# Optimization experiments

Hardware: AMD Instinct MI355X
Metric: run time of the kernel (lower is better)

Reference implementation:

```python
import jax, jax.numpy as jnp
import numpy as np

C = 768; NH = 12; HD = 64; WS = 14; VPT = 10; H0 = 64; B = 8
SCALE = HD ** -0.5


def layernorm(x, w, b, eps=1e-5):
    m = x.mean(-1, keepdims=True)
    v = x.var(-1, keepdims=True)
    return (x - m) / jnp.sqrt(v + eps) * w + b


def setup_inputs() -> dict:
    key = jax.random.key(0)
    ks = jax.random.split(key, 8)
    def rn(k, shape, s=0.02):
        return jax.random.normal(k, shape, jnp.float32) * s
    L = VPT + H0 * H0
    return {
        "x": jax.random.normal(ks[0], (B, L, C), jnp.float32),
        "ln1_w": jnp.ones((C,), jnp.float32),
        "ln1_b": jnp.zeros((C,), jnp.float32),
        "qkv_w": rn(ks[1], (3 * C, C)),
        "qkv_b": jnp.zeros((3 * C,), jnp.float32),
        "proj_w": rn(ks[2], (C, C)),
        "proj_b": jnp.zeros((C,), jnp.float32),
        "rel_pos_h": rn(ks[3], (2 * WS - 1, HD)),
        "rel_pos_w": rn(ks[4], (2 * WS - 1, HD)),
        "ln2_w": jnp.ones((C,), jnp.float32),
        "ln2_b": jnp.zeros((C,), jnp.float32),
        "mlp_w1": rn(ks[5], (4 * C, C)),
        "mlp_b1": jnp.zeros((4 * C,), jnp.float32),
        "mlp_w2": rn(ks[6], (C, 4 * C)),
        "mlp_b2": jnp.zeros((C,), jnp.float32),
        "H": H0,
        "W": H0,
    }


def reference(x, ln1_w, ln1_b, qkv_w, qkv_b, proj_w, proj_b, rel_pos_h, rel_pos_w,
              ln2_w, ln2_b, mlp_w1, mlp_b1, mlp_w2, mlp_b2, H, W):
    B_, L, C_ = x.shape
    shortcut = x
    xn = layernorm(x, ln1_w, ln1_b)

    # --- window partition (SAM style, pad bottom/right) ---
    prompt = xn[:, :VPT]                           # (B, VPT, C)
    sp = xn[:, VPT:].reshape(B_, H, W, C_)
    pad_h = (WS - H % WS) % WS
    pad_w = (WS - W % WS) % WS
    Hp, Wp = H + pad_h, W + pad_w
    sp = jnp.pad(sp, ((0, 0), (0, pad_h), (0, pad_w), (0, 0)))
    nh, nw = Hp // WS, Wp // WS
    win = sp.reshape(B_, nh, WS, nw, WS, C_).transpose(0, 1, 3, 2, 4, 5)
    win = win.reshape(-1, WS * WS, C_)             # (B*nwin, WS*WS, C), batch-major
    nwin = nh * nw
    # faithful to original: prompts broadcast window-major, windows are batch-major
    pr = jnp.broadcast_to(prompt[None], (nwin, B_, VPT, C_)).reshape(-1, VPT, C_)
    tok = jnp.concatenate([pr, win], axis=1)       # (Bw, Lw, C)
    Bw, Lw, _ = tok.shape

    # --- attention with decomposed rel-pos ---
    qkv = tok @ qkv_w.T + qkv_b
    qkv = qkv.reshape(Bw, Lw, 3, NH, HD).transpose(2, 0, 3, 1, 4).reshape(3, Bw * NH, Lw, HD)
    q, k, v = qkv[0], qkv[1], qkv[2]
    attn = (q * SCALE) @ k.transpose(0, 2, 1)      # (Bw*NH, Lw, Lw)

    coords = jnp.arange(WS)[:, None] - jnp.arange(WS)[None, :] + (WS - 1)
    Rh = rel_pos_h[coords]                         # (WS, WS, HD)
    Rw = rel_pos_w[coords]
    rq = q[:, VPT:].reshape(Bw * NH, WS, WS, HD)
    rel_h = jnp.einsum('bhwc,hkc->bhwk', rq, Rh)
    rel_w = jnp.einsum('bhwc,wkc->bhwk', rq, Rw)
    ori = attn[:, VPT:, VPT:].reshape(-1, WS, WS, WS, WS)
    ori = ori + rel_h[:, :, :, :, None] + rel_w[:, :, :, None, :]
    attn = attn.at[:, VPT:, VPT:].set(ori.reshape(-1, WS * WS, WS * WS))

    attn = jax.nn.softmax(attn, axis=-1)
    out = (attn @ v).reshape(Bw, NH, Lw, HD).transpose(0, 2, 1, 3).reshape(Bw, Lw, C_)
    out = out @ proj_w.T + proj_b

    # --- window unpartition ---
    pr_out = out[:, :VPT].reshape(nwin, B_, VPT, C_).mean(0)   # (B, VPT, C)
    wo = out[:, VPT:].reshape(B_, nh, nw, WS, WS, C_).transpose(0, 1, 3, 2, 4, 5)
    wo = wo.reshape(B_, Hp, Wp, C_)[:, :H, :W].reshape(B_, H * W, C_)
    x2 = jnp.concatenate([pr_out, wo], axis=1)

    x2 = shortcut + x2
    h = layernorm(x2, ln2_w, ln2_b)
    h = jax.nn.gelu(h @ mlp_w1.T + mlp_b1, approximate=False)
    x2 = x2 + (h @ mlp_w2.T + mlp_b2)
    return x2
```

## Files before the change

### kernel.cpp

```cpp
#include <hip/hip_runtime.h>
#include <hip/hip_fp16.h>

#define Bb 8
#define Ll 4106
#define Cc 768
#define VPT_ 10
#define WSz 14
#define NWIN 25
#define BW_ 200
#define LW_ 206
#define NHh 12
#define HDd 64

typedef _Float16 half8 __attribute__((ext_vector_type(8)));
typedef float floatx4 __attribute__((ext_vector_type(4)));

__device__ __forceinline__ void gload16(const _Float16* g, _Float16* l) {
    __builtin_amdgcn_global_load_lds(
        (const __attribute__((address_space(1))) void*)g,
        (__attribute__((address_space(3))) void*)l, 16, 0, 0);
}

__global__ void f2h_kernel(const float* __restrict__ in, _Float16* __restrict__ out, int n) {
    int i = blockIdx.x * 256 + threadIdx.x;
    if (i < n) out[i] = (_Float16)in[i];
}

__global__ __launch_bounds__(256) void ln1_kernel(
    const float* __restrict__ x, const float* __restrict__ w, const float* __restrict__ bia,
    _Float16* __restrict__ xn)
{
    int r = blockIdx.x;
    const float* xr = x + (size_t)r * Cc;
    int t = threadIdx.x;
    float v0 = xr[t], v1 = xr[t + 256], v2 = xr[t + 512];
    float s1 = v0 + v1 + v2;
    float s2 = v0 * v0 + v1 * v1 + v2 * v2;
    #pragma unroll
    for (int off = 32; off > 0; off >>= 1) {
        s1 += __shfl_down(s1, off);
        s2 += __shfl_down(s2, off);
    }
    __shared__ float red[8];
    int wv = t >> 6, ln = t & 63;
    if (ln == 0) { red[wv] = s1; red[4 + wv] = s2; }
    __syncthreads();
    float fs1 = red[0] + red[1] + red[2] + red[3];
    float fs2 = red[4] + red[5] + red[6] + red[7];
    float mean = fs1 * (1.0f / Cc);
    float var  = fs2 * (1.0f / Cc) - mean * mean;
    float rstd = rsqrtf(var + 1e-5f);
    float vv[3] = {v0, v1, v2};
    #pragma unroll
    for (int i = 0; i < 3; ++i) {
        int c = t + i * 256;
        xn[(size_t)r * Cc + c] = (_Float16)((vv[i] - mean) * rstd * w[c] + bia[c]);
    }
}

__global__ __launch_bounds__(256) void ln2_kernel(
    const _Float16* __restrict__ x2, const float* __restrict__ w, const float* __restrict__ bia,
    _Float16* __restrict__ xn)
{
    int r = blockIdx.x;
    const _Float16* xr = x2 + (size_t)r * Cc;
    int t = threadIdx.x;
    float v0 = (float)xr[t], v1 = (float)xr[t + 256], v2 = (float)xr[t + 512];
    float s1 = v0 + v1 + v2;
    float s2 = v0 * v0 + v1 * v1 + v2 * v2;
    #pragma unroll
    for (int off = 32; off > 0; off >>= 1) {
        s1 += __shfl_down(s1, off);
        s2 += __shfl_down(s2, off);
    }
    __shared__ float red[8];
    int wv = t >> 6, ln = t & 63;
    if (ln == 0) { red[wv] = s1; red[4 + wv] = s2; }
    __syncthreads();
    float fs1 = red[0] + red[1] + red[2] + red[3];
    float fs2 = red[4] + red[5] + red[6] + red[7];
    float mean = fs1 * (1.0f / Cc);
    float var  = fs2 * (1.0f / Cc) - mean * mean;
    float rstd = rsqrtf(var + 1e-5f);
    float vv[3] = {v0, v1, v2};
    #pragma unroll
    for (int i = 0; i < 3; ++i) {
        int c = t + i * 256;
        xn[(size_t)r * Cc + c] = (_Float16)((vv[i] - mean) * rstd * w[c] + bia[c]);
    }
}

__global__ __launch_bounds__(256) void pmean_kernel(
    const _Float16* __restrict__ attP, _Float16* __restrict__ attS)
{
    int r = blockIdx.x;
    int b = r / VPT_, l = r % VPT_;
    int t = threadIdx.x;
    #pragma unroll
    for (int i = 0; i < 3; ++i) {
        int c = t + i * 256;
        float s = 0.0f;
        for (int wi = 0; wi < NWIN; ++wi)
            s += (float)attP[((size_t)((wi * Bb + b) * VPT_ + l)) * Cc + c];
        attS[((size_t)(b * Ll + l)) * Cc + c] = (_Float16)(s * (1.0f / NWIN));
    }
}

template <int EPI>
__global__ __launch_bounds__(256) void gemm128(
    const _Float16* __restrict__ A, const _Float16* __restrict__ W,
    const float* __restrict__ bias, const _Float16* __restrict__ addsrc,
    const float* __restrict__ addF,
    _Float16* __restrict__ outH, float* __restrict__ outF,
    int M, int N, int K, int gm, int gn)
{
    __shared__ alignas(16) _Float16 As[128 * 32];
    __shared__ alignas(16) _Float16 Bs[128 * 32];

    int pid = blockIdx.x;
    int width = 8 * gn;
    int gid = pid / width;
    int first = gid * 8;
    int gsz = gm - first; if (gsz > 8) gsz = 8;
    int rem = pid - gid * width;
    int pm = first + rem % gsz;
    int pn = rem / gsz;
    int row0 = pm * 128, col0 = pn * 128;

    int tid = threadIdx.x;
    int wv = tid >> 6, ln = tid & 63;
    int n = ln & 15, quad = ln >> 4;
    int wr = wv >> 1, wc = wv & 1;
    int lr = ln >> 2, lg = ln & 3;

    int lsw = (lg ^ ((lr >> 1) & 3)) * 8;
    int ar0 = row0 + wv * 16 + lr;        if (ar0 > M - 1) ar0 = M - 1;
    int ar1 = row0 + (wv + 4) * 16 + lr;  if (ar1 > M - 1) ar1 = M - 1;
    const _Float16* Ap0 = A + (size_t)ar0 * K + lsw;
    const _Float16* Ap1 = A + (size_t)ar1 * K + lsw;
    const _Float16* Bp0 = W + (size_t)(col0 + wv * 16 + lr) * K + lsw;
    const _Float16* Bp1 = W + (size_t)(col0 + (wv + 4) * 16 + lr) * K + lsw;
    _Float16* lA0 = As + wv * 512;
    _Float16* lA1 = As + (wv + 4) * 512;
    _Float16* lB0 = Bs + wv * 512;
    _Float16* lB1 = Bs + (wv + 4) * 512;

    const int cq = (quad ^ ((n >> 1) & 3)) * 8;

    floatx4 acc[4][4] = {};

    for (int k0 = 0; k0 < K; k0 += 32) {
        __syncthreads();
        gload16(Ap0 + k0, lA0);
        gload16(Ap1 + k0, lA1);
        gload16(Bp0 + k0, lB0);
        gload16(Bp1 + k0, lB1);
        __syncthreads();
        half8 af[4], bf[4];
        #pragma unroll
        for (int i = 0; i < 4; ++i)
            af[i] = *reinterpret_cast<const half8*>(&As[(wr * 64 + i * 16 + n) * 32 + cq]);
        #pragma unroll
        for (int j = 0; j < 4; ++j)
            bf[j] = *reinterpret_cast<const half8*>(&Bs[(wc * 64 + j * 16 + n) * 32 + cq]);
        #pragma unroll
        for (int i = 0; i < 4; ++i)
            #pragma unroll
            for (int j = 0; j < 4; ++j)
                acc[i][j] = __builtin_amdgcn_mfma_f32_16x16x32_f16(af[i], bf[j], acc[i][j], 0, 0, 0);
    }

    float bv[4];
    #pragma unroll
    for (int j = 0; j < 4; ++j) bv[j] = bias[col0 + wc * 64 + j * 16 + n];

    if (EPI == 2) {
        #pragma unroll
        for (int i = 0; i < 4; ++i)
            #pragma unroll
            for (int j = 0; j < 4; ++j) {
                int col = col0 + wc * 64 + j * 16 + n;
                #pragma unroll
                for (int rr = 0; rr < 4; ++rr) {
                    int row = row0 + wr * 64 + i * 16 + quad * 4 + rr;
                    if (row < M) {
                        size_t off = (size_t)row * N + col;
                        outF[off] = acc[i][j][rr] + bv[j] + (float)addsrc[off];
                    }
                }
            }
    } else if (EPI == 3) {
        #pragma unroll
        for (int i = 0; i < 4; ++i)
            #pragma unroll
            for (int j = 0; j < 4; ++j) {
                int col = col0 + wc * 64 + j * 16 + n;
                #pragma unroll
                for (int rr = 0; rr < 4; ++rr) {
                    int row = row0 + wr * 64 + i * 16 + quad * 4 + rr;
                    if (row < M) {
                        size_t off = (size_t)row * N + col;
                        outH[off] = (_Float16)(acc[i][j][rr] + bv[j] + addF[off]);
                    }
                }
            }
    } else {
        __syncthreads();
        _Float16* Tb = (wv < 2 ? As : Bs) + (wv & 1) * 2048;
        #pragma unroll
        for (int i = 0; i < 4; ++i) {
            #pragma unroll
            for (int j = 0; j < 4; ++j)
                #pragma unroll
                for (int rr = 0; rr < 4; ++rr) {
                    float v = acc[i][j][rr] + bv[j];
                    if (EPI == 1) v = 0.5f * v * (1.0f + erff(v * 0.70710678118654752f));
                    Tb[(quad * 4 + rr) * 72 + j * 16 + n] = (_Float16)v;
                }
            __syncthreads();
            int row = row0 + wr * 64 + i * 16 + lr;
            if (row < M) {
                uint4 p0 = *reinterpret_cast<const uint4*>(&Tb[lr * 72 + lg * 8]);
                uint4 p1 = *reinterpret_cast<const uint4*>(&Tb[lr * 72 + 32 + lg * 8]);
                _Float16* po = outH + (size_t)row * N + col0 + wc * 64 + lg * 8;
                *reinterpret_cast<uint4*>(po) = p0;
                *reinterpret_cast<uint4*>(po + 32) = p1;
            }
        }
    }
}

__global__ __launch_bounds__(256, 2) void attn_mfma_kernel(
    const _Float16* __restrict__ qkv, const _Float16* __restrict__ qkvbh,
    const float* __restrict__ relh, const float* __restrict__ relw,
    _Float16* __restrict__ attS, _Float16* __restrict__ attP)
{
    __shared__ alignas(16) _Float16 Ks[208 * 72];
    __shared__ alignas(16) _Float16 Vt[64 * 232];
    __shared__ alignas(16) _Float16 Pc[4][16 * 40];
    __shared__ alignas(16) float    Tabs[4][896];
    __shared__ int rowOff[208];
    const int bwi = blockIdx.x / NHh, hh = blockIdx.x % NHh;
    const int tid = threadIdx.x;

    const int bp = bwi & 7;
    const int bs = bwi / NWIN;
    const int wis = bwi % NWIN;
    const int wh = wis / 5, ww = wis % 5;

    const int wv = tid >> 6, ln = tid & 63;
    const int n = ln & 15, quad = ln >> 4;

    if (tid < 208) {
        int row = tid, off = -1;
        if (row < VPT_) off = bp * Ll + row;
        else if (row < LW_) {
            int s = row - VPT_;
            int i = s / WSz, j = s - i * WSz;
            int gi = wh * WSz + i, gj = ww * WSz + j;
            if (gi < 64 && gj < 64) off = bs * Ll + VPT_ + gi * 64 + gj;
        }
        rowOff[row] = off;
    }

    half8 bh[2][2], bwf[2][2];
    #pragma unroll
    for (int ct = 0; ct < 2; ++ct) {
        int j = ct * 16 + n; if (j > 26) j = 26;
        #pragma unroll
        for (int kk = 0; kk < 2; ++kk) {
            const float* ph = relh + j * 64 + kk * 32 + quad * 8;
            const float* pw = relw + j * 64 + kk * 32 + quad * 8;
            half8 hf, wf;
            #pragma unroll
            for (int e = 0; e < 8; ++e) { hf[e] = (_Float16)ph[e]; wf[e] = (_Float16)pw[e]; }
            bh[ct][kk] = hf; bwf[ct][kk] = wf;
        }
    }

    int khv[13], kwv[13];
    #pragma unroll
    for (int ct = 0; ct < 13; ++ct) {
        int key = ct * 16 + n;
        int k2 = key - VPT_; if (k2 < 0) k2 = 0;
        khv[ct] = k2 / WSz; kwv[ct] = k2 - khv[ct] * WSz;
    }
    __syncthreads();

    half8 qa0, qa1;
    {
        int qrow = wv * 16 + n; if (qrow > 205) qrow = 205;
        int ro = rowOff[qrow];
        const _Float16* qp = (ro >= 0 ? qkv + (size_t)ro * 2304 : qkvbh) + hh * HDd + quad * 8;
        qa0 = *reinterpret_cast<const half8*>(qp);
        qa1 = *reinterpret_cast<const half8*>(qp + 32);
    }

    for (int idx = tid; idx < LW_ * 8; idx += 256) {
        int row = idx >> 3, c8 = idx & 7;
        int ro = rowOff[row];
        const _Float16* src = (ro >= 0 ? qkv + (size_t)ro * 2304 : qkvbh) + 768 + hh * HDd;
        *reinterpret_cast<uint4*>(&Ks[row * 72 + c8 * 8]) =
            *reinterpret_cast<const uint4*>(src + c8 * 8);
    }
    for (int idx = tid; idx < LW_ * 64; idx += 256) {
        int row = idx >> 6, d = idx & 63;
        int ro = rowOff[row];
        const _Float16* src = (ro >= 0 ? qkv + (size_t)ro * 2304 : qkvbh) + 1536 + hh * HDd;
        Vt[d * 232 + row] = src[d];
    }
    for (int idx = tid; idx < 64 * 26; idx += 256) {
        int d = idx / 26, c = idx - d * 26;
        Vt[d * 232 + 206 + c] = (_Float16)0.0f;
    }
    __syncthreads();

    float* tw_t = Tabs[wv];
    float* th_t = Tabs[wv] + 448;
    _Float16* pcw = &Pc[wv][0];

    for (int rt = wv; rt < 13; rt += 4) {
        int nrt = rt + 4; if (nrt > 12) nrt = 12;
        int nqrow = nrt * 16 + n; if (nqrow > 205) nqrow = 205;
        int nro = rowOff[nqrow];
        const _Float16* nqp = (nro >= 0 ? qkv + (size_t)nro * 2304 : qkvbh) + hh * HDd + quad * 8;
        half8 nq0 = *reinterpret_cast<const half8*>(nqp);
        half8 nq1 = *reinterpret_cast<const half8*>(nqp + 32);

        floatx4 th0 = {}, th1 = {}, tw0 = {}, tw1 = {};
        th0 = __builtin_amdgcn_mfma_f32_16x16x32_f16(qa0, bh[0][0], th0, 0, 0, 0);
        th0 = __builtin_amdgcn_mfma_f32_16x16x32_f16(qa1, bh[0][1], th0, 0, 0, 0);
        th1 = __builtin_amdgcn_mfma_f32_16x16x32_f16(qa0, bh[1][0], th1, 0, 0, 0);
        th1 = __builtin_amdgcn_mfma_f32_16x16x32_f16(qa1, bh[1][1], th1, 0, 0, 0);
        tw0 = __builtin_amdgcn_mfma_f32_16x16x32_f16(qa0, bwf[0][0], tw0, 0, 0, 0);
        tw0 = __builtin_amdgcn_mfma_f32_16x16x32_f16(qa1, bwf[0][1], tw0, 0, 0, 0);
        tw1 = __builtin_amdgcn_mfma_f32_16x16x32_f16(qa0, bwf[1][0], tw1, 0, 0, 0);
        tw1 = __builtin_amdgcn_mfma_f32_16x16x32_f16(qa1, bwf[1][1], tw1, 0, 0, 0);

        #pragma unroll
        for (int rr = 0; rr < 4; ++rr) {
            int lrow = quad * 4 + rr;
            th_t[lrow * 28 + n] = th0[rr];
            tw_t[lrow * 28 + n] = tw0[rr];
            if (n < 12) {
                th_t[lrow * 28 + 16 + n] = th1[rr];
                tw_t[lrow * 28 + 16 + n] = tw1[rr];
            }
        }

        floatx4 s[13];
        #pragma unroll
        for (int ct = 0; ct < 13; ++ct) {
            half8 kb0 = *reinterpret_cast<const half8*>(&Ks[(ct * 16 + n) * 72 + quad * 8]);
            half8 kb1 = *reinterpret_cast<const half8*>(&Ks[(ct * 16 + n) * 72 + 32 + quad * 8]);
            floatx4 a = {};
            a = __builtin_amdgcn_mfma_f32_16x16x32_f16(qa0, kb0, a, 0, 0, 0);
            a = __builtin_amdgcn_mfma_f32_16x16x32_f16(qa1, kb1, a, 0, 0, 0);
            s[ct] = a;
        }

        #pragma unroll
        for (int rr = 0; rr < 4; ++rr) {
            int row = rt * 16 + quad * 4 + rr;
            bool rowok = (row >= VPT_) && (row < LW_);
            int q2 = row - VPT_; if (q2 < 0) q2 = 0;
            int qh = q2 / WSz, qw = q2 - qh * WSz;
            const float* thr = th_t + (quad * 4 + rr) * 28;
            const float* twr = tw_t + (quad * 4 + rr) * 28;
            #pragma unroll
            for (int ct = 0; ct < 13; ++ct) {
                int key = ct * 16 + n;
                float tv = thr[qh - khv[ct] + 13] + twr[qw - kwv[ct] + 13];
                float sv = s[ct][rr] * 0.125f;
                sv += (rowok && key >= VPT_ && key < LW_) ? tv : 0.0f;
                if (key >= LW_) sv = -1e30f;
                s[ct][rr] = sv;
            }
        }

        float mx[4] = {-1e30f, -1e30f, -1e30f, -1e30f};
        #pragma unroll
        for (int ct = 0; ct < 13; ++ct)
            #pragma unroll
            for (int rr = 0; rr < 4; ++rr) mx[rr] = fmaxf(mx[rr], s[ct][rr]);
        #pragma unroll
        for (int rr = 0; rr < 4; ++rr)
            #pragma unroll
            for (int off = 1; off < 16; off <<= 1) mx[rr] = fmaxf(mx[rr], __shfl_xor(mx[rr], off));
        float sm[4] = {0.f, 0.f, 0.f, 0.f};
        #pragma unroll
        for (int ct = 0; ct < 13; ++ct)
            #pragma unroll
            for (int rr = 0; rr < 4; ++rr) {
                float p = __expf(s[ct][rr] - mx[rr]);
                s[ct][rr] = p; sm[rr] += p;
            }
        #pragma unroll
        for (int rr = 0; rr < 4; ++rr) {
            #pragma unroll
            for (int off = 1; off < 16; off <<= 1) sm[rr] += __shfl_xor(sm[rr], off);
            sm[rr] = 1.0f / sm[rr];
        }
        #pragma unroll
        for (int ct = 0; ct < 13; ++ct)
            #pragma unroll
            for (int rr = 0; rr < 4; ++rr) s[ct][rr] *= sm[rr];

        floatx4 o[4] = {};
        #pragma unroll
        for (int kt = 0; kt < 7; ++kt) {
            #pragma unroll
            for (int h2 = 0; h2 < 2; ++h2) {
                int ct = kt * 2 + h2;
                #pragma unroll
                for (int rr = 0; rr < 4; ++rr) {
                    float pv = (ct < 13) ? s[ct][rr] : 0.0f;
                    pcw[(quad * 4 + rr) * 40 + h2 * 16 + n] = (_Float16)pv;
                }
            }
            half8 pa = *reinterpret_cast<const half8*>(&pcw[n * 40 + quad * 8]);
            #pragma unroll
            for (int dt = 0; dt < 4; ++dt) {
                half8 vb = *reinterpret_cast<const half8*>(&Vt[(dt * 16 + n) * 232 + kt * 32 + quad * 8]);
                o[dt] = __builtin_amdgcn_mfma_f32_16x16x32_f16(pa, vb, o[dt], 0, 0, 0);
            }
        }

        #pragma unroll
        for (int dt = 0; dt < 4; ++dt)
            #pragma unroll
            for (int rr = 0; rr < 4; ++rr) {
                int row = rt * 16 + quad * 4 + rr;
                if (row >= LW_) continue;
                _Float16 val = (_Float16)o[dt][rr];
                int col = hh * HDd + dt * 16 + n;
                if (row < VPT_) {
                    attP[((size_t)(bwi * VPT_ + row)) * Cc + col] = val;
                } else {
                    int g = rowOff[row];
                    if (g >= 0) attS[(size_t)g * Cc + col] = val;
                }
            }

        qa0 = nq0; qa1 = nq1;
    }
}

extern "C" void kernel_launch(void* const* d_in, const int* in_sizes, int n_in,
                              void* d_out, int out_size, void* d_ws, size_t ws_size,
                              hipStream_t stream)
{
    const float* x     = (const float*)d_in[0];
    const float* ln1w  = (const float*)d_in[1];
    const float* ln1b  = (const float*)d_in[2];
    const float* qkvw  = (const float*)d_in[3];
    const float* qkvb  = (const float*)d_in[4];
    const float* projw = (const float*)d_in[5];
    const float* projb = (const float*)d_in[6];
    const float* relh  = (const float*)d_in[7];
    const float* relw  = (const float*)d_in[8];
    const float* ln2w  = (const float*)d_in[9];
    const float* ln2b  = (const float*)d_in[10];
    const float* w1    = (const float*)d_in[11];
    const float* b1    = (const float*)d_in[12];
    const float* w2    = (const float*)d_in[13];
    const float* b2    = (const float*)d_in[14];
    float* out = (float*)d_out;
    char* ws = (char*)d_ws;

    _Float16* wqkv_h  = (_Float16*)(ws + 0);
    _Float16* wproj_h = (_Float16*)(ws + 3538944);
    _Float16* w1_h    = (_Float16*)(ws + 4718592);
    _Float16* w2_h    = (_Float16*)(ws + 9437184);
    _Float16* qkvb_h  = (_Float16*)(ws + 14155776);
    _Float16* attP    = (_Float16*)(ws + 14160384);
    _Float16* tokA    = (_Float16*)(ws + 17232384);
    char* regB = ws + 77438976;
    _Float16* qkv_h  = (_Float16*)regB;
    _Float16* hbuf   = (_Float16*)regB;
    _Float16* x2h    = (_Float16*)(regB + 100909056);

    f2h_kernel<<<(2304 * 768 + 255) / 256, 256, 0, stream>>>(qkvw, wqkv_h, 2304 * 768);
    f2h_kernel<<<(768 * 768 + 255) / 256, 256, 0, stream>>>(projw, wproj_h, 768 * 768);
    f2h_kernel<<<(3072 * 768 + 255) / 256, 256, 0, stream>>>(w1, w1_h, 3072 * 768);
    f2h_kernel<<<(768 * 3072 + 255) / 256, 256, 0, stream>>>(w2, w2_h, 768 * 3072);
    f2h_kernel<<<9, 256, 0, stream>>>(qkvb, qkvb_h, 2304);
    ln1_kernel<<<Bb * Ll, 256, 0, stream>>>(x, ln1w, ln1b, tokA);
    gemm128<0><<<257 * 18, 256, 0, stream>>>(tokA, wqkv_h, qkvb, nullptr, nullptr, qkv_h, nullptr,
                                             32848, 2304, 768, 257, 18);
    attn_mfma_kernel<<<BW_ * NHh, 256, 0, stream>>>(qkv_h, qkvb_h, relh, relw, tokA, attP);
    pmean_kernel<<<Bb * VPT_, 256, 0, stream>>>(attP, tokA);
    gemm128<3><<<257 * 6, 256, 0, stream>>>(tokA, wproj_h, projb, nullptr, x, x2h, nullptr,
                                            32848, 768, 768, 257, 6);
    ln2_kernel<<<Bb * Ll, 256, 0, stream>>>(x2h, ln2w, ln2b, tokA);
    for (int ch = 0; ch < 2; ++ch) {
        size_t r0 = (size_t)ch * 16424;
        gemm128<1><<<129 * 24, 256, 0, stream>>>(tokA + r0 * 768, w1_h, b1, nullptr, nullptr, hbuf, nullptr,
                                                 16424, 3072, 768, 129, 24);
        gemm128<2><<<129 * 6, 256, 0, stream>>>(hbuf, w2_h, b2, x2h + r0 * 768, nullptr, nullptr, out + r0 * 768,
                                                16424, 768, 3072, 129, 6);
    }
}
```

Before: 1.402 ms.

## Replace 128x128 GEMM with double-buffered 256x256 tile, 512-thread kernel

The GEMM moves from 128x128x32 tiles on 256 threads to 256x256x64 tiles on 512 threads, with double-buffered LDS (128 KB total) so the next K-slice is loaded while the current one is computed. Each wave now holds a 128x64 accumulator, which raises arithmetic intensity and halves the barriers per K. The cost is one block per CU, higher register pressure, and fewer blocks for the N=768 GEMMs (387 and 195 blocks), which can leave CUs idle and cause tail imbalance.

```diff
diff --git a/kernel.cpp b/kernel.cpp
--- a/kernel.cpp
+++ b/kernel.cpp
@@ -107,15 +107,14 @@
 }
 
 template <int EPI>
-__global__ __launch_bounds__(256) void gemm128(
+__global__ __launch_bounds__(512, 1) void gemm256(
     const _Float16* __restrict__ A, const _Float16* __restrict__ W,
     const float* __restrict__ bias, const _Float16* __restrict__ addsrc,
     const float* __restrict__ addF,
     _Float16* __restrict__ outH, float* __restrict__ outF,
     int M, int N, int K, int gm, int gn)
 {
-    __shared__ alignas(16) _Float16 As[128 * 32];
-    __shared__ alignas(16) _Float16 Bs[128 * 32];
+    __shared__ alignas(16) _Float16 AB[2][2][256 * 64];
 
     int pid = blockIdx.x;
     int width = 8 * gn;
@@ -125,64 +124,83 @@
     int rem = pid - gid * width;
     int pm = first + rem % gsz;
     int pn = rem / gsz;
-    int row0 = pm * 128, col0 = pn * 128;
+    int row0 = pm * 256, col0 = pn * 256;
 
     int tid = threadIdx.x;
     int wv = tid >> 6, ln = tid & 63;
     int n = ln & 15, quad = ln >> 4;
-    int wr = wv >> 1, wc = wv & 1;
+    int wm = wv >> 2, wn = wv & 3;
     int lr = ln >> 2, lg = ln & 3;
 
-    int lsw = (lg ^ ((lr >> 1) & 3)) * 8;
-    int ar0 = row0 + wv * 16 + lr;        if (ar0 > M - 1) ar0 = M - 1;
-    int ar1 = row0 + (wv + 4) * 16 + lr;  if (ar1 > M - 1) ar1 = M - 1;
-    const _Float16* Ap0 = A + (size_t)ar0 * K + lsw;
-    const _Float16* Ap1 = A + (size_t)ar1 * K + lsw;
-    const _Float16* Bp0 = W + (size_t)(col0 + wv * 16 + lr) * K + lsw;
-    const _Float16* Bp1 = W + (size_t)(col0 + (wv + 4) * 16 + lr) * K + lsw;
-    _Float16* lA0 = As + wv * 512;
-    _Float16* lA1 = As + (wv + 4) * 512;
-    _Float16* lB0 = Bs + wv * 512;
-    _Float16* lB1 = Bs + (wv + 4) * 512;
-
-    const int cq = (quad ^ ((n >> 1) & 3)) * 8;
-
-    floatx4 acc[4][4] = {};
-
-    for (int k0 = 0; k0 < K; k0 += 32) {
+    const _Float16* gAp[4];
+    const _Float16* gBp[4];
+    #pragma unroll
+    for (int i = 0; i < 4; ++i) {
+        int slot = i * 512 + tid;
+        int r = slot >> 3, p = slot & 7;
+        int c = (p ^ (r & 7)) * 8;
+        int ar = row0 + r; if (ar > M - 1) ar = M - 1;
+        gAp[i] = A + (size_t)ar * K + c;
+        gBp[i] = W + (size_t)(col0 + r) * K + c;
+    }
+    const int c0 = (quad ^ (n & 7)) * 8;
+    const int c1 = ((4 + quad) ^ (n & 7)) * 8;
+
+    floatx4 acc[8][4] = {};
+
+    const int nt = K >> 6;
+    int cur = 0;
+    #pragma unroll
+    for (int i = 0; i < 4; ++i) {
+        gload16(gAp[i], &AB[0][0][i * 4096 + wv * 512]);
+        gload16(gBp[i], &AB[0][1][i * 4096 + wv * 512]);
+    }
+    __syncthreads();
+
+    for (int t = 0; t < nt; ++t) {
+        if (t + 1 < nt) {
+            int k0 = (t + 1) << 6;
+            #pragma unroll
+            for (int i = 0; i < 4; ++i) {
+                gload16(gAp[i] + k0, &AB[cur ^ 1][0][i * 4096 + wv * 512]);
+                gload16(gBp[i] + k0, &AB[cur ^ 1][1][i * 4096 + wv * 512]);
+            }
+        }
+        const _Float16* Alds = &AB[cur][0][0] + (wm * 128 + n) * 64;
+        const _Float16* Blds = &AB[cur][1][0] + (wn * 64 + n) * 64;
+        half8 bf[4][2];
+        #pragma unroll
+        for (int j = 0; j < 4; ++j) {
+            bf[j][0] = *reinterpret_cast<const half8*>(Blds + j * 1024 + c0);
+            bf[j][1] = *reinterpret_cast<const half8*>(Blds + j * 1024 + c1);
+        }
+        #pragma unroll
+        for (int i = 0; i < 8; ++i) {
+            half8 a0 = *reinterpret_cast<const half8*>(Alds + i * 1024 + c0);
+            half8 a1 = *reinterpret_cast<const half8*>(Alds + i * 1024 + c1);
+            #pragma unroll
+            for (int j = 0; j < 4; ++j) {
+                acc[i][j] = __builtin_amdgcn_mfma_f32_16x16x32_f16(a0, bf[j][0], acc[i][j], 0, 0, 0);
+                acc[i][j] = __builtin_amdgcn_mfma_f32_16x16x32_f16(a1, bf[j][1], acc[i][j], 0, 0, 0);
+            }
+        }
         __syncthreads();
-        gload16(Ap0 + k0, lA0);
-        gload16(Ap1 + k0, lA1);
-        gload16(Bp0 + k0, lB0);
-        gload16(Bp1 + k0, lB1);
-        __syncthreads();
-        half8 af[4], bf[4];
-        #pragma unroll
-        for (int i = 0; i < 4; ++i)
-            af[i] = *reinterpret_cast<const half8*>(&As[(wr * 64 + i * 16 + n) * 32 + cq]);
-        #pragma unroll
-        for (int j = 0; j < 4; ++j)
-            bf[j] = *reinterpret_cast<const half8*>(&Bs[(wc * 64 + j * 16 + n) * 32 + cq]);
-        #pragma unroll
-        for (int i = 0; i < 4; ++i)
-            #pragma unroll
-            for (int j = 0; j < 4; ++j)
-                acc[i][j] = __builtin_amdgcn_mfma_f32_16x16x32_f16(af[i], bf[j], acc[i][j], 0, 0, 0);
+        cur ^= 1;
     }
 
     float bv[4];
     #pragma unroll
-    for (int j = 0; j < 4; ++j) bv[j] = bias[col0 + wc * 64 + j * 16 + n];
+    for (int j = 0; j < 4; ++j) bv[j] = bias[col0 + wn * 64 + j * 16 + n];
 
     if (EPI == 2) {
         #pragma unroll
-        for (int i = 0; i < 4; ++i)
+        for (int i = 0; i < 8; ++i)
             #pragma unroll
             for (int j = 0; j < 4; ++j) {
-                int col = col0 + wc * 64 + j * 16 + n;
+                int col = col0 + wn * 64 + j * 16 + n;
                 #pragma unroll
                 for (int rr = 0; rr < 4; ++rr) {
-                    int row = row0 + wr * 64 + i * 16 + quad * 4 + rr;
+                    int row = row0 + wm * 128 + i * 16 + quad * 4 + rr;
                     if (row < M) {
                         size_t off = (size_t)row * N + col;
                         outF[off] = acc[i][j][rr] + bv[j] + (float)addsrc[off];
@@ -191,13 +209,13 @@
             }
     } else if (EPI == 3) {
         #pragma unroll
-        for (int i = 0; i < 4; ++i)
+        for (int i = 0; i < 8; ++i)
             #pragma unroll
             for (int j = 0; j < 4; ++j) {
-                int col = col0 + wc * 64 + j * 16 + n;
+                int col = col0 + wn * 64 + j * 16 + n;
                 #pragma unroll
                 for (int rr = 0; rr < 4; ++rr) {
-                    int row = row0 + wr * 64 + i * 16 + quad * 4 + rr;
+                    int row = row0 + wm * 128 + i * 16 + quad * 4 + rr;
                     if (row < M) {
                         size_t off = (size_t)row * N + col;
                         outH[off] = (_Float16)(acc[i][j][rr] + bv[j] + addF[off]);
@@ -205,10 +223,9 @@
                 }
             }
     } else {
-        __syncthreads();
-        _Float16* Tb = (wv < 2 ? As : Bs) + (wv & 1) * 2048;
-        #pragma unroll
-        for (int i = 0; i < 4; ++i) {
+        _Float16* Tb = &AB[0][0][0] + wv * 1152;
+        #pragma unroll
+        for (int i = 0; i < 8; ++i) {
             #pragma unroll
             for (int j = 0; j < 4; ++j)
                 #pragma unroll
@@ -218,11 +235,11 @@
                     Tb[(quad * 4 + rr) * 72 + j * 16 + n] = (_Float16)v;
                 }
             __syncthreads();
-            int row = row0 + wr * 64 + i * 16 + lr;
+            int row = row0 + wm * 128 + i * 16 + lr;
             if (row < M) {
                 uint4 p0 = *reinterpret_cast<const uint4*>(&Tb[lr * 72 + lg * 8]);
                 uint4 p1 = *reinterpret_cast<const uint4*>(&Tb[lr * 72 + 32 + lg * 8]);
-                _Float16* po = outH + (size_t)row * N + col0 + wc * 64 + lg * 8;
+                _Float16* po = outH + (size_t)row * N + col0 + wn * 64 + lg * 8;
                 *reinterpret_cast<uint4*>(po) = p0;
                 *reinterpret_cast<uint4*>(po + 32) = p1;
             }
@@ -486,18 +503,18 @@
     f2h_kernel<<<(768 * 3072 + 255) / 256, 256, 0, stream>>>(w2, w2_h, 768 * 3072);
     f2h_kernel<<<9, 256, 0, stream>>>(qkvb, qkvb_h, 2304);
     ln1_kernel<<<Bb * Ll, 256, 0, stream>>>(x, ln1w, ln1b, tokA);
-    gemm128<0><<<257 * 18, 256, 0, stream>>>(tokA, wqkv_h, qkvb, nullptr, nullptr, qkv_h, nullptr,
-                                             32848, 2304, 768, 257, 18);
+    gemm256<0><<<129 * 9, 512, 0, stream>>>(tokA, wqkv_h, qkvb, nullptr, nullptr, qkv_h, nullptr,
+                                            32848, 2304, 768, 129, 9);
     attn_mfma_kernel<<<BW_ * NHh, 256, 0, stream>>>(qkv_h, qkvb_h, relh, relw, tokA, attP);
     pmean_kernel<<<Bb * VPT_, 256, 0, stream>>>(attP, tokA);
-    gemm128<3><<<257 * 6, 256, 0, stream>>>(tokA, wproj_h, projb, nullptr, x, x2h, nullptr,
-                                            32848, 768, 768, 257, 6);
+    gemm256<3><<<129 * 3, 512, 0, stream>>>(tokA, wproj_h, projb, nullptr, x, x2h, nullptr,
+                                            32848, 768, 768, 129, 3);
     ln2_kernel<<<Bb * Ll, 256, 0, stream>>>(x2h, ln2w, ln2b, tokA);
     for (int ch = 0; ch < 2; ++ch) {
         size_t r0 = (size_t)ch * 16424;
-        gemm128<1><<<129 * 24, 256, 0, stream>>>(tokA + r0 * 768, w1_h, b1, nullptr, nullptr, hbuf, nullptr,
-                                                 16424, 3072, 768, 129, 24);
-        gemm128<2><<<129 * 6, 256, 0, stream>>>(hbuf, w2_h, b2, x2h + r0 * 768, nullptr, nullptr, out + r0 * 768,
-                                                16424, 768, 3072, 129, 6);
-    }
-}
+        gemm256<1><<<65 * 12, 512, 0, stream>>>(tokA + r0 * 768, w1_h, b1, nullptr, nullptr, hbuf, nullptr,
+                                                16424, 3072, 768, 65, 12);
+        gemm256<2><<<65 * 3, 512, 0, stream>>>(hbuf, w2_h, b2, x2h + r0 * 768, nullptr, nullptr, out + r0 * 768,
+                                               16424, 768, 3072, 65, 3);
+    }
+}
```

Result: faster. 1.232 ms (-12.1%).
